# Performance work log

Measured on AMD Instinct MI355X. Metric: run time of the kernel, lower is better.

Reference implementation:

```python
import jax, jax.numpy as jnp
import numpy as np

EPS = 1e-6

def _l2normalize(x, axis=1):
    # matches torch: x / sqrt(sum(x^2) + eps)
    norm = jnp.sqrt(jnp.sum(x * x, axis=axis, keepdims=True) + EPS)
    return x / norm


def setup_inputs() -> dict:
    key = jax.random.key(0)
    k1, k2, k3 = jax.random.split(key, 3)
    B, C, H, W = 8, 64, 48, 48
    x = jax.random.normal(k1, (B, C, H, W), dtype=jnp.float32)
    v = jax.random.normal(k2, (B, C, H, W), dtype=jnp.float32)
    pos = jax.random.normal(k3, (B, C, H, W), dtype=jnp.float32)
    # learned scalar parameters (init values from the torch module)
    gamma = jnp.float32(0.0)
    beta_gamma = jnp.float32(10.0)
    sum_gamma0 = jnp.float32(0.0)
    sum_gamma1 = jnp.float32(0.0)
    return {"x": x, "v": v, "pos": pos, "gamma": gamma,
            "beta_gamma": beta_gamma, "sum_gamma0": sum_gamma0,
            "sum_gamma1": sum_gamma1}


def reference(x, v, pos, gamma, beta_gamma, sum_gamma0, sum_gamma1):
    B, C, H, W = x.shape
    N = H * W
    # q and k are computed identically in the original module; compute once.
    q = _l2normalize(x + gamma * pos, axis=1)          # [B, C, H, W]
    qf = q.reshape(B, C, N)                             # [B, C, N]
    vf = v.reshape(B, v.shape[1], N)                    # [B, Cv, N]
    # scores[b, n, m] = <q[:, n], k[:, m]>; learned temperature beta_gamma
    scores = jnp.einsum('bcn,bcm->bnm', qf, qf) * beta_gamma  # [B, N, N]
    beta = jax.nn.softmax(scores, axis=-1)              # [B, N, N]
    # o = v @ beta^T  => o[b, c, n] = sum_m v[b, c, m] * beta[b, n, m]
    o = jnp.einsum('bcm,bnm->bcn', vf, beta).reshape(B, vf.shape[1], H, W)
    e0 = jnp.exp(sum_gamma0)
    e1 = jnp.exp(sum_gamma1)
    tot = e0 + e1
    out = (e0 / tot) * o + (e1 / tot) * v
    return out, beta.reshape(B, N, H, W)
```

## Files before the change

### kernel.cpp

```cpp
#include <hip/hip_runtime.h>
#include <hip/hip_bf16.h>

#define B_  8
#define C_  64
#define N_  2304
#define TS  64
#define NT_ (N_ / TS)
#define LDP 72
#define SPL 4
#define MTS (NT_ / SPL)

typedef __attribute__((ext_vector_type(8))) short  short8;
typedef __attribute__((ext_vector_type(4))) float  floatx4;

struct Hdr { int f32mode; float gamma, bg, cmax, w0, w1; };

__device__ __forceinline__ float bf2f(unsigned short u) {
  return __uint_as_float(((unsigned int)u) << 16);
}
__device__ __forceinline__ unsigned short f2bf(float f) {
  unsigned int x = __float_as_uint(f);
  x += 0x7fff + ((x >> 16) & 1);
  return (unsigned short)(x >> 16);
}

__global__ void detect_k(const void* g, const void* bgp, const void* s0,
                         const void* s1, Hdr* h) {
  if (threadIdx.x == 0 && blockIdx.x == 0) {
    int f32 = (((const unsigned short*)bgp)[0] == 0) ? 1 : 0;
    float gamma, bg, sg0, sg1;
    if (f32) {
      gamma = ((const float*)g)[0];  bg  = ((const float*)bgp)[0];
      sg0   = ((const float*)s0)[0]; sg1 = ((const float*)s1)[0];
    } else {
      gamma = bf2f(((const unsigned short*)g)[0]);
      bg    = bf2f(((const unsigned short*)bgp)[0]);
      sg0   = bf2f(((const unsigned short*)s0)[0]);
      sg1   = bf2f(((const unsigned short*)s1)[0]);
    }
    float e0 = __expf(sg0), e1 = __expf(sg1);
    h->f32mode = f32;
    h->gamma = gamma;
    h->bg = bg;
    h->cmax = fabsf(bg);
    h->w0 = e0 / (e0 + e1);
    h->w1 = e1 / (e0 + e1);
  }
}

__global__ __launch_bounds__(64)
void prep_q(const void* __restrict__ xv, const void* __restrict__ posv,
            const Hdr* __restrict__ h, unsigned short* __restrict__ qT) {
  int t = blockIdx.x * 64 + threadIdx.x;
  int b = t / N_;
  int n = t - b * N_;
  const bool f32 = h->f32mode;
  float gamma = h->gamma;
  float vals[C_];
  float s = 0.f;
  if (f32) {
    const float* xp = (const float*)xv  + (size_t)b * C_ * N_ + n;
    const float* pp = (const float*)posv + (size_t)b * C_ * N_ + n;
#pragma unroll
    for (int c = 0; c < C_; ++c) {
      float val = xp[(size_t)c * N_] + gamma * pp[(size_t)c * N_];
      vals[c] = val;  s += val * val;
    }
  } else {
    const unsigned short* xp = (const unsigned short*)xv  + (size_t)b * C_ * N_ + n;
    const unsigned short* pp = (const unsigned short*)posv + (size_t)b * C_ * N_ + n;
#pragma unroll
    for (int c = 0; c < C_; ++c) {
      float val = bf2f(xp[(size_t)c * N_]) + gamma * bf2f(pp[(size_t)c * N_]);
      vals[c] = val;  s += val * val;
    }
  }
  float inv = rsqrtf(s + 1e-6f);
  unsigned int* qrow = reinterpret_cast<unsigned int*>(qT + (size_t)t * C_);
#pragma unroll
  for (int c = 0; c < C_; c += 2) {
    qrow[c >> 1] = (unsigned int)f2bf(vals[c] * inv)
                 | ((unsigned int)f2bf(vals[c + 1] * inv) << 16);
  }
}

__global__ __launch_bounds__(256)
void pass1_rowsum(const unsigned short* __restrict__ qT,
                  const void* __restrict__ vraw,
                  const Hdr* __restrict__ h,
                  unsigned short* __restrict__ vb,
                  float* __restrict__ rowsum_part) {
  int bx  = blockIdx.x;
  int tid = threadIdx.x;
  {
    int t = bx * 256 + tid;
    unsigned int* vb32 = reinterpret_cast<unsigned int*>(vb);
    if (h->f32mode) {
      const float* vf = (const float*)vraw;
#pragma unroll
      for (int k = 0; k < 2; ++k) {
        int i = t + k * 294912;
        float f0 = vf[2 * i], f1 = vf[2 * i + 1];
        vb32[i] = (unsigned int)f2bf(f0) | ((unsigned int)f2bf(f1) << 16);
      }
    } else {
      const unsigned int* v32 = (const unsigned int*)vraw;
#pragma unroll
      for (int k = 0; k < 2; ++k) {
        int i = t + k * 294912;
        vb32[i] = v32[i];
      }
    }
  }
  int s  = bx & (SPL - 1);
  int nt = (bx >> 2) % NT_;
  int b  = bx / (SPL * NT_);
  int n0 = nt * TS;
  int wave = tid >> 6;
  int lane = tid & 63;
  int quad = lane >> 4;
  int l15  = lane & 15;
  float bg = h->bg, cmax = h->cmax;
  const unsigned short* abase =
      qT + ((size_t)(b * N_ + n0 + 16 * wave + l15)) * C_ + quad * 8;
  short8 a0 = *reinterpret_cast<const short8*>(abase);
  short8 a1 = *reinterpret_cast<const short8*>(abase + 32);
  float acc[4] = {0.f, 0.f, 0.f, 0.f};
  int mt0 = s * MTS;
  for (int mt = mt0; mt < mt0 + MTS; ++mt) {
    int m0 = mt * TS;
#pragma unroll
    for (int j = 0; j < 4; ++j) {
      const unsigned short* qb =
          qT + ((size_t)(b * N_ + m0 + j * 16 + l15)) * C_ + quad * 8;
      short8 b0 = *reinterpret_cast<const short8*>(qb);
      short8 b1 = *reinterpret_cast<const short8*>(qb + 32);
      floatx4 d = {0.f, 0.f, 0.f, 0.f};
      d = __builtin_amdgcn_mfma_f32_16x16x32_bf16(a0, b0, d, 0, 0, 0);
      d = __builtin_amdgcn_mfma_f32_16x16x32_bf16(a1, b1, d, 0, 0, 0);
#pragma unroll
      for (int r = 0; r < 4; ++r)
        acc[r] += __expf(d[r] * bg - cmax);
    }
  }
#pragma unroll
  for (int r = 0; r < 4; ++r) {
    float vv = acc[r];
    vv += __shfl_xor(vv, 1);
    vv += __shfl_xor(vv, 2);
    vv += __shfl_xor(vv, 4);
    vv += __shfl_xor(vv, 8);
    acc[r] = vv;
  }
  if (l15 == 0) {
#pragma unroll
    for (int r = 0; r < 4; ++r)
      rowsum_part[((size_t)(b * N_ + n0 + 16 * wave + quad * 4 + r)) * SPL + s]
          = acc[r];
  }
}

__global__ __launch_bounds__(256)
void pass2_attn(const unsigned short* __restrict__ qT,
                const unsigned short* __restrict__ vb,
                const Hdr* __restrict__ h,
                const float* __restrict__ rowsum_part,
                float* __restrict__ opart,
                void* __restrict__ dout) {
  __shared__ unsigned short pt[2][TS * LDP];
  int bx = blockIdx.x;
  int s  = bx & (SPL - 1);
  int nt = (bx >> 2) % NT_;
  int b  = bx / (SPL * NT_);
  int n0 = nt * TS;
  int tid  = threadIdx.x;
  int wave = tid >> 6;
  int lane = tid & 63;
  int quad = lane >> 4;
  int l15  = lane & 15;
  const bool f32 = h->f32mode;
  float bg = h->bg, cmax = h->cmax;
  unsigned short* out16  = (unsigned short*)dout;
  unsigned short* beta16 = out16 + (size_t)B_ * C_ * N_;
  float* beta32 = (float*)dout + (size_t)B_ * C_ * N_;

  const unsigned short* abase =
      qT + ((size_t)(b * N_ + n0 + 16 * wave + l15)) * C_ + quad * 8;
  short8 a0 = *reinterpret_cast<const short8*>(abase);
  short8 a1 = *reinterpret_cast<const short8*>(abase + 32);
  float inv[4];
#pragma unroll
  for (int r = 0; r < 4; ++r) {
    floatx4 rs = *reinterpret_cast<const floatx4*>(
        rowsum_part + ((size_t)(b * N_ + n0 + 16 * wave + quad * 4 + r)) * SPL);
    inv[r] = 1.f / (rs[0] + rs[1] + rs[2] + rs[3]);
  }
  floatx4 oacc[4] = {{0.f,0.f,0.f,0.f},{0.f,0.f,0.f,0.f},
                     {0.f,0.f,0.f,0.f},{0.f,0.f,0.f,0.f}};
  int mtb = s * MTS;
  const unsigned short* vrow = vb + ((size_t)(b * C_ + 16 * wave + l15)) * N_;
  for (int it = 0; it < MTS; ++it) {
    int m0 = (mtb + it) * TS;
    unsigned short* ptc = pt[it & 1];
    short8 av0 = *reinterpret_cast<const short8*>(vrow + m0 + quad * 8);
    short8 av1 = *reinterpret_cast<const short8*>(vrow + m0 + 32 + quad * 8);
#pragma unroll
    for (int j = 0; j < 4; ++j) {
      const unsigned short* qb =
          qT + ((size_t)(b * N_ + m0 + j * 16 + l15)) * C_ + quad * 8;
      short8 b0 = *reinterpret_cast<const short8*>(qb);
      short8 b1 = *reinterpret_cast<const short8*>(qb + 32);
      floatx4 d = {0.f, 0.f, 0.f, 0.f};
      d = __builtin_amdgcn_mfma_f32_16x16x32_bf16(a0, b0, d, 0, 0, 0);
      d = __builtin_amdgcn_mfma_f32_16x16x32_bf16(a1, b1, d, 0, 0, 0);
#pragma unroll
      for (int r = 0; r < 4; ++r) {
        float p = __expf(d[r] * bg - cmax) * inv[r];
        ptc[(16 * wave + quad * 4 + r) * LDP + j * 16 + l15] = f2bf(p);
        if (f32) {
          beta32[((size_t)(b * N_ + n0 + 16 * wave + quad * 4 + r)) * N_
                 + m0 + j * 16 + l15] = p;
        }
      }
    }
    asm volatile("s_waitcnt lgkmcnt(0)" ::: "memory");
    __builtin_amdgcn_s_barrier();
    __builtin_amdgcn_sched_barrier(0);
    if (!f32) {
#pragma unroll
      for (int k = 0; k < 2; ++k) {
        int chunk = tid + 256 * k;
        int row = chunk >> 3;
        int col = (chunk & 7) * 8;
        short8 pv = *reinterpret_cast<const short8*>(&ptc[row * LDP + col]);
        *reinterpret_cast<short8*>(
            beta16 + ((size_t)(b * N_ + n0 + row)) * N_ + m0 + col) = pv;
      }
    }
#pragma unroll
    for (int j = 0; j < 4; ++j) {
      short8 bp0 = *reinterpret_cast<const short8*>(&ptc[(j * 16 + l15) * LDP + quad * 8]);
      short8 bp1 = *reinterpret_cast<const short8*>(&ptc[(j * 16 + l15) * LDP + 32 + quad * 8]);
      oacc[j] = __builtin_amdgcn_mfma_f32_16x16x32_bf16(av0, bp0, oacc[j], 0, 0, 0);
      oacc[j] = __builtin_amdgcn_mfma_f32_16x16x32_bf16(av1, bp1, oacc[j], 0, 0, 0);
    }
  }
  float* op = opart + (size_t)s * (B_ * C_ * N_);
#pragma unroll
  for (int j = 0; j < 4; ++j) {
#pragma unroll
    for (int r = 0; r < 4; ++r) {
      int c = 16 * wave + quad * 4 + r;
      int n = n0 + 16 * j + l15;
      op[((size_t)(b * C_ + c)) * N_ + n] = oacc[j][r];
    }
  }
}

__global__ __launch_bounds__(256)
void blend_k(const float* __restrict__ opart, const void* __restrict__ vraw,
             const Hdr* __restrict__ h, void* __restrict__ dout) {
  int t = blockIdx.x * 256 + threadIdx.x;
  const int STR = (B_ * C_ * N_) / 4;
  const floatx4* p = reinterpret_cast<const floatx4*>(opart);
  floatx4 o  = p[t];
  floatx4 o1 = p[t + STR];
  floatx4 o2 = p[t + 2 * STR];
  floatx4 o3 = p[t + 3 * STR];
#pragma unroll
  for (int k = 0; k < 4; ++k) o[k] = (o[k] + o1[k]) + (o2[k] + o3[k]);
  float w0 = h->w0, w1 = h->w1;
  if (h->f32mode) {
    floatx4 vv = reinterpret_cast<const floatx4*>(vraw)[t];
    floatx4 r;
#pragma unroll
    for (int k = 0; k < 4; ++k) r[k] = w0 * o[k] + w1 * vv[k];
    reinterpret_cast<floatx4*>(dout)[t] = r;
  } else {
    unsigned long long v64 =
        reinterpret_cast<const unsigned long long*>(vraw)[t];
    unsigned long long rr = 0;
#pragma unroll
    for (int k = 0; k < 4; ++k) {
      float vf = bf2f((unsigned short)(v64 >> (16 * k)));
      rr |= ((unsigned long long)f2bf(w0 * o[k] + w1 * vf)) << (16 * k);
    }
    reinterpret_cast<unsigned long long*>(dout)[t] = rr;
  }
}

extern "C" void kernel_launch(void* const* d_in, const int* in_sizes, int n_in,
                              void* d_out, int out_size, void* d_ws, size_t ws_size,
                              hipStream_t stream) {
  const void* x     = d_in[0];
  const void* v     = d_in[1];
  const void* pos   = d_in[2];
  const void* gamma = d_in[3];
  const void* bg    = d_in[4];
  const void* sg0   = d_in[5];
  const void* sg1   = d_in[6];

  char* ws = (char*)d_ws;
  Hdr* hdr = (Hdr*)ws;
  unsigned short* qT = (unsigned short*)(ws + 256);
  unsigned short* vb = qT + (size_t)B_ * N_ * C_;
  float* rowsum_part = (float*)(ws + 256 + (size_t)B_ * N_ * C_ * 4);
  float* opart = rowsum_part + (size_t)B_ * N_ * SPL;

  detect_k<<<dim3(1), dim3(64), 0, stream>>>(gamma, bg, sg0, sg1, hdr);
  prep_q<<<dim3((B_ * N_) / 64), dim3(64), 0, stream>>>(x, pos, hdr, qT);
  pass1_rowsum<<<dim3(B_ * NT_ * SPL), dim3(256), 0, stream>>>(qT, v, hdr, vb, rowsum_part);
  pass2_attn<<<dim3(B_ * NT_ * SPL), dim3(256), 0, stream>>>(qT, vb, hdr, rowsum_part, opart, d_out);
  blend_k<<<dim3((B_ * C_ * N_) / 1024), dim3(256), 0, stream>>>(opart, v, hdr, d_out);
}
```

Baseline: 276.8 us.

## Stage key and value tiles through double-buffered LDS and drop param-detect kernel

Pass1 and pass2 now stage each 64-row key tile (and in pass2 the value tile) into double-buffered shared memory with coalesced loads. The next tile's global load is issued before the current tile's MFMAs. This replaces the per-lane strided global reads done inside the MFMA loops, and the pass2 beta staging buffer becomes single-buffered with an extra barrier per iteration. The separate detect_k kernel is removed and every kernel recomputes the scalar parameters inline, saving one launch at the cost of redundant scalar loads per thread.

```diff
diff --git a/kernel.cpp b/kernel.cpp
--- a/kernel.cpp
+++ b/kernel.cpp
@@ -13,8 +13,6 @@
 typedef __attribute__((ext_vector_type(8))) short  short8;
 typedef __attribute__((ext_vector_type(4))) float  floatx4;
 
-struct Hdr { int f32mode; float gamma, bg, cmax, w0, w1; };
-
 __device__ __forceinline__ float bf2f(unsigned short u) {
   return __uint_as_float(((unsigned int)u) << 16);
 }
@@ -24,41 +22,49 @@
   return (unsigned short)(x >> 16);
 }
 
-__global__ void detect_k(const void* g, const void* bgp, const void* s0,
-                         const void* s1, Hdr* h) {
-  if (threadIdx.x == 0 && blockIdx.x == 0) {
-    int f32 = (((const unsigned short*)bgp)[0] == 0) ? 1 : 0;
-    float gamma, bg, sg0, sg1;
-    if (f32) {
-      gamma = ((const float*)g)[0];  bg  = ((const float*)bgp)[0];
-      sg0   = ((const float*)s0)[0]; sg1 = ((const float*)s1)[0];
-    } else {
-      gamma = bf2f(((const unsigned short*)g)[0]);
-      bg    = bf2f(((const unsigned short*)bgp)[0]);
-      sg0   = bf2f(((const unsigned short*)s0)[0]);
-      sg1   = bf2f(((const unsigned short*)s1)[0]);
-    }
-    float e0 = __expf(sg0), e1 = __expf(sg1);
-    h->f32mode = f32;
-    h->gamma = gamma;
-    h->bg = bg;
-    h->cmax = fabsf(bg);
-    h->w0 = e0 / (e0 + e1);
-    h->w1 = e1 / (e0 + e1);
-  }
+#define LGKM_BARRIER() do {                                   \
+    asm volatile("s_waitcnt lgkmcnt(0)" ::: "memory");        \
+    __builtin_amdgcn_s_barrier();                             \
+    __builtin_amdgcn_sched_barrier(0);                        \
+  } while (0)
+
+struct Params { int f32; float gamma, bg, cmax, w0, w1; };
+
+__device__ __forceinline__ Params load_params(const void* g, const void* bgp,
+                                              const void* s0, const void* s1) {
+  Params p;
+  p.f32 = (((const unsigned short*)bgp)[0] == 0) ? 1 : 0;
+  float sg0, sg1;
+  if (p.f32) {
+    p.gamma = ((const float*)g)[0];
+    p.bg    = ((const float*)bgp)[0];
+    sg0     = ((const float*)s0)[0];
+    sg1     = ((const float*)s1)[0];
+  } else {
+    p.gamma = bf2f(((const unsigned short*)g)[0]);
+    p.bg    = bf2f(((const unsigned short*)bgp)[0]);
+    sg0     = bf2f(((const unsigned short*)s0)[0]);
+    sg1     = bf2f(((const unsigned short*)s1)[0]);
+  }
+  float e0 = __expf(sg0), e1 = __expf(sg1);
+  p.cmax = fabsf(p.bg);
+  p.w0 = e0 / (e0 + e1);
+  p.w1 = e1 / (e0 + e1);
+  return p;
 }
 
 __global__ __launch_bounds__(64)
 void prep_q(const void* __restrict__ xv, const void* __restrict__ posv,
-            const Hdr* __restrict__ h, unsigned short* __restrict__ qT) {
+            const void* g, const void* bgp, const void* s0p, const void* s1p,
+            unsigned short* __restrict__ qT) {
+  Params hp = load_params(g, bgp, s0p, s1p);
   int t = blockIdx.x * 64 + threadIdx.x;
   int b = t / N_;
   int n = t - b * N_;
-  const bool f32 = h->f32mode;
-  float gamma = h->gamma;
+  float gamma = hp.gamma;
   float vals[C_];
   float s = 0.f;
-  if (f32) {
+  if (hp.f32) {
     const float* xp = (const float*)xv  + (size_t)b * C_ * N_ + n;
     const float* pp = (const float*)posv + (size_t)b * C_ * N_ + n;
 #pragma unroll
@@ -87,15 +93,17 @@
 __global__ __launch_bounds__(256)
 void pass1_rowsum(const unsigned short* __restrict__ qT,
                   const void* __restrict__ vraw,
-                  const Hdr* __restrict__ h,
+                  const void* g, const void* bgp, const void* s0p, const void* s1p,
                   unsigned short* __restrict__ vb,
                   float* __restrict__ rowsum_part) {
+  __shared__ unsigned short qm[2][TS * LDP];
+  Params hp = load_params(g, bgp, s0p, s1p);
   int bx  = blockIdx.x;
   int tid = threadIdx.x;
   {
     int t = bx * 256 + tid;
     unsigned int* vb32 = reinterpret_cast<unsigned int*>(vb);
-    if (h->f32mode) {
+    if (hp.f32) {
       const float* vf = (const float*)vraw;
 #pragma unroll
       for (int k = 0; k < 2; ++k) {
@@ -120,21 +128,42 @@
   int lane = tid & 63;
   int quad = lane >> 4;
   int l15  = lane & 15;
-  float bg = h->bg, cmax = h->cmax;
+  float bg = hp.bg, cmax = hp.cmax;
+  int srow0 = tid >> 3;
+  int srow1 = srow0 + 32;
+  int scol  = (tid & 7) * 8;
   const unsigned short* abase =
       qT + ((size_t)(b * N_ + n0 + 16 * wave + l15)) * C_ + quad * 8;
   short8 a0 = *reinterpret_cast<const short8*>(abase);
   short8 a1 = *reinterpret_cast<const short8*>(abase + 32);
+  int mt0 = s * MTS;
+  {
+    int m0 = mt0 * TS;
+    short8 r0 = *reinterpret_cast<const short8*>(
+        qT + ((size_t)(b * N_ + m0 + srow0)) * C_ + scol);
+    short8 r1 = *reinterpret_cast<const short8*>(
+        qT + ((size_t)(b * N_ + m0 + srow1)) * C_ + scol);
+    *reinterpret_cast<short8*>(&qm[0][srow0 * LDP + scol]) = r0;
+    *reinterpret_cast<short8*>(&qm[0][srow1 * LDP + scol]) = r1;
+  }
+  LGKM_BARRIER();
   float acc[4] = {0.f, 0.f, 0.f, 0.f};
-  int mt0 = s * MTS;
-  for (int mt = mt0; mt < mt0 + MTS; ++mt) {
-    int m0 = mt * TS;
+  int cur = 0;
+  for (int it = 0; it < MTS; ++it) {
+    short8 r0 = {0,0,0,0,0,0,0,0}, r1 = {0,0,0,0,0,0,0,0};
+    bool more = (it + 1 < MTS);
+    if (more) {
+      int m1 = (mt0 + it + 1) * TS;
+      r0 = *reinterpret_cast<const short8*>(
+          qT + ((size_t)(b * N_ + m1 + srow0)) * C_ + scol);
+      r1 = *reinterpret_cast<const short8*>(
+          qT + ((size_t)(b * N_ + m1 + srow1)) * C_ + scol);
+    }
+    const unsigned short* qc = qm[cur];
 #pragma unroll
     for (int j = 0; j < 4; ++j) {
-      const unsigned short* qb =
-          qT + ((size_t)(b * N_ + m0 + j * 16 + l15)) * C_ + quad * 8;
-      short8 b0 = *reinterpret_cast<const short8*>(qb);
-      short8 b1 = *reinterpret_cast<const short8*>(qb + 32);
+      short8 b0 = *reinterpret_cast<const short8*>(&qc[(j * 16 + l15) * LDP + quad * 8]);
+      short8 b1 = *reinterpret_cast<const short8*>(&qc[(j * 16 + l15) * LDP + 32 + quad * 8]);
       floatx4 d = {0.f, 0.f, 0.f, 0.f};
       d = __builtin_amdgcn_mfma_f32_16x16x32_bf16(a0, b0, d, 0, 0, 0);
       d = __builtin_amdgcn_mfma_f32_16x16x32_bf16(a1, b1, d, 0, 0, 0);
@@ -142,6 +171,13 @@
       for (int r = 0; r < 4; ++r)
         acc[r] += __expf(d[r] * bg - cmax);
     }
+    if (more) {
+      unsigned short* qn = qm[cur ^ 1];
+      *reinterpret_cast<short8*>(&qn[srow0 * LDP + scol]) = r0;
+      *reinterpret_cast<short8*>(&qn[srow1 * LDP + scol]) = r1;
+    }
+    LGKM_BARRIER();
+    cur ^= 1;
   }
 #pragma unroll
   for (int r = 0; r < 4; ++r) {
@@ -163,11 +199,14 @@
 __global__ __launch_bounds__(256)
 void pass2_attn(const unsigned short* __restrict__ qT,
                 const unsigned short* __restrict__ vb,
-                const Hdr* __restrict__ h,
+                const void* g, const void* bgp, const void* s0p, const void* s1p,
                 const float* __restrict__ rowsum_part,
                 float* __restrict__ opart,
                 void* __restrict__ dout) {
-  __shared__ unsigned short pt[2][TS * LDP];
+  __shared__ unsigned short qm[2][TS * LDP];
+  __shared__ unsigned short vt[2][TS * LDP];
+  __shared__ unsigned short pt[TS * LDP];
+  Params hp = load_params(g, bgp, s0p, s1p);
   int bx = blockIdx.x;
   int s  = bx & (SPL - 1);
   int nt = (bx >> 2) % NT_;
@@ -178,11 +217,15 @@
   int lane = tid & 63;
   int quad = lane >> 4;
   int l15  = lane & 15;
-  const bool f32 = h->f32mode;
-  float bg = h->bg, cmax = h->cmax;
+  const bool f32 = hp.f32;
+  float bg = hp.bg, cmax = hp.cmax;
   unsigned short* out16  = (unsigned short*)dout;
   unsigned short* beta16 = out16 + (size_t)B_ * C_ * N_;
   float* beta32 = (float*)dout + (size_t)B_ * C_ * N_;
+
+  int srow0 = tid >> 3;
+  int srow1 = srow0 + 32;
+  int scol  = (tid & 7) * 8;
 
   const unsigned short* abase =
       qT + ((size_t)(b * N_ + n0 + 16 * wave + l15)) * C_ + quad * 8;
@@ -198,52 +241,89 @@
   floatx4 oacc[4] = {{0.f,0.f,0.f,0.f},{0.f,0.f,0.f,0.f},
                      {0.f,0.f,0.f,0.f},{0.f,0.f,0.f,0.f}};
   int mtb = s * MTS;
-  const unsigned short* vrow = vb + ((size_t)(b * C_ + 16 * wave + l15)) * N_;
+  {
+    int m0 = mtb * TS;
+    short8 q0 = *reinterpret_cast<const short8*>(
+        qT + ((size_t)(b * N_ + m0 + srow0)) * C_ + scol);
+    short8 q1 = *reinterpret_cast<const short8*>(
+        qT + ((size_t)(b * N_ + m0 + srow1)) * C_ + scol);
+    short8 v0 = *reinterpret_cast<const short8*>(
+        vb + ((size_t)(b * C_ + srow0)) * N_ + m0 + scol);
+    short8 v1 = *reinterpret_cast<const short8*>(
+        vb + ((size_t)(b * C_ + srow1)) * N_ + m0 + scol);
+    *reinterpret_cast<short8*>(&qm[0][srow0 * LDP + scol]) = q0;
+    *reinterpret_cast<short8*>(&qm[0][srow1 * LDP + scol]) = q1;
+    *reinterpret_cast<short8*>(&vt[0][srow0 * LDP + scol]) = v0;
+    *reinterpret_cast<short8*>(&vt[0][srow1 * LDP + scol]) = v1;
+  }
+  LGKM_BARRIER();
+  int cur = 0;
   for (int it = 0; it < MTS; ++it) {
     int m0 = (mtb + it) * TS;
-    unsigned short* ptc = pt[it & 1];
-    short8 av0 = *reinterpret_cast<const short8*>(vrow + m0 + quad * 8);
-    short8 av1 = *reinterpret_cast<const short8*>(vrow + m0 + 32 + quad * 8);
+    bool more = (it + 1 < MTS);
+    short8 q0r = {0,0,0,0,0,0,0,0}, q1r = {0,0,0,0,0,0,0,0};
+    short8 v0r = {0,0,0,0,0,0,0,0}, v1r = {0,0,0,0,0,0,0,0};
+    if (more) {
+      int m1 = m0 + TS;
+      q0r = *reinterpret_cast<const short8*>(
+          qT + ((size_t)(b * N_ + m1 + srow0)) * C_ + scol);
+      q1r = *reinterpret_cast<const short8*>(
+          qT + ((size_t)(b * N_ + m1 + srow1)) * C_ + scol);
+      v0r = *reinterpret_cast<const short8*>(
+          vb + ((size_t)(b * C_ + srow0)) * N_ + m1 + scol);
+      v1r = *reinterpret_cast<const short8*>(
+          vb + ((size_t)(b * C_ + srow1)) * N_ + m1 + scol);
+    }
+    const unsigned short* qc = qm[cur];
 #pragma unroll
     for (int j = 0; j < 4; ++j) {
-      const unsigned short* qb =
-          qT + ((size_t)(b * N_ + m0 + j * 16 + l15)) * C_ + quad * 8;
-      short8 b0 = *reinterpret_cast<const short8*>(qb);
-      short8 b1 = *reinterpret_cast<const short8*>(qb + 32);
+      short8 b0 = *reinterpret_cast<const short8*>(&qc[(j * 16 + l15) * LDP + quad * 8]);
+      short8 b1 = *reinterpret_cast<const short8*>(&qc[(j * 16 + l15) * LDP + 32 + quad * 8]);
       floatx4 d = {0.f, 0.f, 0.f, 0.f};
       d = __builtin_amdgcn_mfma_f32_16x16x32_bf16(a0, b0, d, 0, 0, 0);
       d = __builtin_amdgcn_mfma_f32_16x16x32_bf16(a1, b1, d, 0, 0, 0);
 #pragma unroll
       for (int r = 0; r < 4; ++r) {
         float p = __expf(d[r] * bg - cmax) * inv[r];
-        ptc[(16 * wave + quad * 4 + r) * LDP + j * 16 + l15] = f2bf(p);
+        pt[(16 * wave + quad * 4 + r) * LDP + j * 16 + l15] = f2bf(p);
         if (f32) {
           beta32[((size_t)(b * N_ + n0 + 16 * wave + quad * 4 + r)) * N_
                  + m0 + j * 16 + l15] = p;
         }
       }
     }
-    asm volatile("s_waitcnt lgkmcnt(0)" ::: "memory");
-    __builtin_amdgcn_s_barrier();
-    __builtin_amdgcn_sched_barrier(0);
+    LGKM_BARRIER();
+    if (more) {
+      unsigned short* qn = qm[cur ^ 1];
+      unsigned short* vn = vt[cur ^ 1];
+      *reinterpret_cast<short8*>(&qn[srow0 * LDP + scol]) = q0r;
+      *reinterpret_cast<short8*>(&qn[srow1 * LDP + scol]) = q1r;
+      *reinterpret_cast<short8*>(&vn[srow0 * LDP + scol]) = v0r;
+      *reinterpret_cast<short8*>(&vn[srow1 * LDP + scol]) = v1r;
+    }
     if (!f32) {
 #pragma unroll
       for (int k = 0; k < 2; ++k) {
         int chunk = tid + 256 * k;
         int row = chunk >> 3;
         int col = (chunk & 7) * 8;
-        short8 pv = *reinterpret_cast<const short8*>(&ptc[row * LDP + col]);
+        short8 pv = *reinterpret_cast<const short8*>(&pt[row * LDP + col]);
         *reinterpret_cast<short8*>(
             beta16 + ((size_t)(b * N_ + n0 + row)) * N_ + m0 + col) = pv;
       }
     }
+    const unsigned short* vc = vt[cur];
+    short8 av0 = *reinterpret_cast<const short8*>(&vc[(16 * wave + l15) * LDP + quad * 8]);
+    short8 av1 = *reinterpret_cast<const short8*>(&vc[(16 * wave + l15) * LDP + 32 + quad * 8]);
 #pragma unroll
     for (int j = 0; j < 4; ++j) {
-      short8 bp0 = *reinterpret_cast<const short8*>(&ptc[(j * 16 + l15) * LDP + quad * 8]);
-      short8 bp1 = *reinterpret_cast<const short8*>(&ptc[(j * 16 + l15) * LDP + 32 + quad * 8]);
+      short8 bp0 = *reinterpret_cast<const short8*>(&pt[(j * 16 + l15) * LDP + quad * 8]);
+      short8 bp1 = *reinterpret_cast<const short8*>(&pt[(j * 16 + l15) * LDP + 32 + quad * 8]);
       oacc[j] = __builtin_amdgcn_mfma_f32_16x16x32_bf16(av0, bp0, oacc[j], 0, 0, 0);
       oacc[j] = __builtin_amdgcn_mfma_f32_16x16x32_bf16(av1, bp1, oacc[j], 0, 0, 0);
     }
+    LGKM_BARRIER();
+    cur ^= 1;
   }
   float* op = opart + (size_t)s * (B_ * C_ * N_);
 #pragma unroll
@@ -259,7 +339,9 @@
 
 __global__ __launch_bounds__(256)
 void blend_k(const float* __restrict__ opart, const void* __restrict__ vraw,
-             const Hdr* __restrict__ h, void* __restrict__ dout) {
+             const void* g, const void* bgp, const void* s0p, const void* s1p,
+             void* __restrict__ dout) {
+  Params hp = load_params(g, bgp, s0p, s1p);
   int t = blockIdx.x * 256 + threadIdx.x;
   const int STR = (B_ * C_ * N_) / 4;
   const floatx4* p = reinterpret_cast<const floatx4*>(opart);
@@ -269,8 +351,8 @@
   floatx4 o3 = p[t + 3 * STR];
 #pragma unroll
   for (int k = 0; k < 4; ++k) o[k] = (o[k] + o1[k]) + (o2[k] + o3[k]);
-  float w0 = h->w0, w1 = h->w1;
-  if (h->f32mode) {
+  float w0 = hp.w0, w1 = hp.w1;
+  if (hp.f32) {
     floatx4 vv = reinterpret_cast<const floatx4*>(vraw)[t];
     floatx4 r;
 #pragma unroll
@@ -301,15 +383,17 @@
   const void* sg1   = d_in[6];
 
   char* ws = (char*)d_ws;
-  Hdr* hdr = (Hdr*)ws;
   unsigned short* qT = (unsigned short*)(ws + 256);
   unsigned short* vb = qT + (size_t)B_ * N_ * C_;
   float* rowsum_part = (float*)(ws + 256 + (size_t)B_ * N_ * C_ * 4);
   float* opart = rowsum_part + (size_t)B_ * N_ * SPL;
 
-  detect_k<<<dim3(1), dim3(64), 0, stream>>>(gamma, bg, sg0, sg1, hdr);
-  prep_q<<<dim3((B_ * N_) / 64), dim3(64), 0, stream>>>(x, pos, hdr, qT);
-  pass1_rowsum<<<dim3(B_ * NT_ * SPL), dim3(256), 0, stream>>>(qT, v, hdr, vb, rowsum_part);
-  pass2_attn<<<dim3(B_ * NT_ * SPL), dim3(256), 0, stream>>>(qT, vb, hdr, rowsum_part, opart, d_out);
-  blend_k<<<dim3((B_ * C_ * N_) / 1024), dim3(256), 0, stream>>>(opart, v, hdr, d_out);
-}
+  prep_q<<<dim3((B_ * N_) / 64), dim3(64), 0, stream>>>(
+      x, pos, gamma, bg, sg0, sg1, qT);
+  pass1_rowsum<<<dim3(B_ * NT_ * SPL), dim3(256), 0, stream>>>(
+      qT, v, gamma, bg, sg0, sg1, vb, rowsum_part);
+  pass2_attn<<<dim3(B_ * NT_ * SPL), dim3(256), 0, stream>>>(
+      qT, vb, gamma, bg, sg0, sg1, rowsum_part, opart, d_out);
+  blend_k<<<dim3((B_ * C_ * N_) / 1024), dim3(256), 0, stream>>>(
+      opart, v, gamma, bg, sg0, sg1, d_out);
+}
```

After: 233.3 us. 1.19x faster.
